# Kernel optimization log

Measured on AMD Instinct MI355X. Metric: run time of the kernel, lower is better.

Reference implementation:

```python
import jax, jax.numpy as jnp
import numpy as np

H = 8
D = 512
DK = D // H
B = 16
N = 8192


def setup_inputs() -> dict:
    key = jax.random.key(0)
    k1, k2, k3, k4 = jax.random.split(key, 4)
    x = jax.random.normal(k1, (B, N, D), dtype=jnp.float32)
    W_k = jax.random.normal(k2, (D, D), dtype=jnp.float32) * (1.0 / np.sqrt(D))
    W_g = jax.random.normal(k3, (D, D), dtype=jnp.float32) * (1.0 / np.sqrt(D))
    query = jax.random.normal(k4, (H, 1, DK), dtype=jnp.float32)
    return {"x": x, "W_k": W_k, "W_g": W_g, "query": query}


def reference(x, W_k, W_g, query):
    b, n, d = x.shape
    # nn.Linear: y = x @ W.T  (no bias)
    K = (x @ W_k.T).reshape(b, n, H, DK).transpose(0, 2, 1, 3)  # (b,h,n,dk)
    G = (x @ W_g.T).reshape(b, n, H, DK).transpose(0, 2, 1, 3)  # (b,h,n,dk)
    xh = x.reshape(b, n, H, DK).transpose(0, 2, 1, 3)           # (b,h,n,dk)
    gated = jnp.tanh(K) * jax.nn.sigmoid(G)                     # (b,h,n,dk)
    # single-query attention: scores (b,h,1,n)
    scores = jnp.einsum('hmd,bhnd->bhmn', query, gated)
    attn = jax.nn.softmax(scores, axis=-1)
    out = jnp.einsum('bhmn,bhnd->bhmd', attn, xh)               # (b,h,1,dk)
    out = out.transpose(0, 2, 1, 3).reshape(b, 1, H * DK)
    return out.squeeze()  # (b, d)
```

## Files before the change

### kernel.cpp

```cpp
#include <hip/hip_runtime.h>
#include <hip/hip_bf16.h>

#define H_ 8
#define D_ 512
#define DK_ 64
#define B_ 16
#define N_ 8192
#define M_ (B_ * N_)

typedef __attribute__((ext_vector_type(8))) short short8;
typedef __attribute__((ext_vector_type(4))) float floatx4;

__device__ __forceinline__ void glds16(const void* g, void* l) {
    __builtin_amdgcn_global_load_lds((const __attribute__((address_space(1))) void*)g,
                                     (__attribute__((address_space(3))) void*)l,
                                     16, 0, 0);
}

__device__ __forceinline__ unsigned short f2bf(float f) {
    unsigned u = __float_as_uint(f);
    return (unsigned short)((u + 0x7fffu + ((u >> 16) & 1u)) >> 16);
}

__device__ __forceinline__ unsigned cvt_pk(float lo, float hi) {
    unsigned r;
    asm("v_cvt_pk_bf16_f32 %0, %1, %2" : "=v"(r) : "v"(lo), "v"(hi));
    return r;
}

__device__ __forceinline__ short8 pack_bf8(float4 lo, float4 hi) {
    union { unsigned u[4]; short8 s; } tmp;
    tmp.u[0] = cvt_pk(lo.x, lo.y);
    tmp.u[1] = cvt_pk(lo.z, lo.w);
    tmp.u[2] = cvt_pk(hi.x, hi.y);
    tmp.u[3] = cvt_pk(hi.z, hi.w);
    return tmp.s;
}

#define NX4_ ((M_ * D_) / 4)
#define NW4_ ((D_ * D_) / 4)
__global__ __launch_bounds__(256) void cvt3_kernel(
    const float* __restrict__ x, const float* __restrict__ wk, const float* __restrict__ wg,
    unsigned short* __restrict__ xb, unsigned short* __restrict__ wkb, unsigned short* __restrict__ wgb) {
    int i = blockIdx.x * blockDim.x + threadIdx.x;
    const int stride = gridDim.x * blockDim.x;
    const int total = NX4_ + 2 * NW4_;
    for (; i < total; i += stride) {
        const float4* src;
        ushort4* dst;
        if (i < NX4_)              { src = (const float4*)x  + i;             dst = (ushort4*)xb  + i; }
        else if (i < NX4_ + NW4_)  { src = (const float4*)wk + (i - NX4_);    dst = (ushort4*)wkb + (i - NX4_); }
        else                       { src = (const float4*)wg + (i - NX4_ - NW4_); dst = (ushort4*)wgb + (i - NX4_ - NW4_); }
        float4 v = *src;
        ushort4 o;
        o.x = f2bf(v.x); o.y = f2bf(v.y); o.z = f2bf(v.z); o.w = f2bf(v.w);
        *dst = o;
    }
}

__global__ __launch_bounds__(256) void cvt_kernel(const float* __restrict__ src,
                                                  unsigned short* __restrict__ dst, int n4) {
    int i = blockIdx.x * blockDim.x + threadIdx.x;
    int stride = gridDim.x * blockDim.x;
    for (; i < n4; i += stride) {
        float4 v = ((const float4*)src)[i];
        ushort4 o;
        o.x = f2bf(v.x); o.y = f2bf(v.y); o.z = f2bf(v.z); o.w = f2bf(v.w);
        ((ushort4*)dst)[i] = o;
    }
}

__global__ __launch_bounds__(256, 2) void gemm_score_kernel(
    const unsigned short* __restrict__ xb,
    const unsigned short* __restrict__ wkb,
    const unsigned short* __restrict__ wgb,
    const float* __restrict__ query,
    float* __restrict__ s_buf)
{
    __shared__ __attribute__((aligned(16))) unsigned short lds_a[2][128 * 64];
    __shared__ __attribute__((aligned(16))) unsigned short lds_k[128 * 64];
    __shared__ __attribute__((aligned(16))) unsigned short lds_g[128 * 64];

    const int t = threadIdx.x;
    const int lane = t & 63;
    const int wave = t >> 6;
    const int wm = wave >> 1, wn = wave & 1;
    const int fr = lane & 15;
    const int q4 = lane >> 4;
    const int sw = fr & 7;

    const int g = blockIdx.x;
    const int xcd = g & 7;
    const int s = g >> 3;
    const int jt = s & 3;
    const int mt = ((s >> 2) << 3) | xcd;
    const int jc = jt * 128;
    const int m0 = mt * 128;

    size_t aoff[4];
    int boff[4];
#pragma unroll
    for (int i = 0; i < 4; ++i) {
        int p = i * 256 + t;
        int r = p >> 3;
        int c = (p & 7) ^ (r & 7);
        aoff[i] = (size_t)(m0 + r) * 512 + c * 8;
        boff[i] = (jc + r) * 512 + c * 8;
    }

    floatx4 acc_k[4][4], acc_g[4][4];
#pragma unroll
    for (int i = 0; i < 4; ++i)
#pragma unroll
        for (int j = 0; j < 4; ++j) { acc_k[i][j] = (floatx4)0.f; acc_g[i][j] = (floatx4)0.f; }

#pragma unroll
    for (int i = 0; i < 4; ++i)
        glds16(xb + aoff[i], &lds_a[0][(size_t)(i * 256 + t) * 8]);
#pragma unroll
    for (int i = 0; i < 4; ++i) {
        glds16(wkb + boff[i], lds_k + (size_t)(i * 256 + t) * 8);
        glds16(wgb + boff[i], lds_g + (size_t)(i * 256 + t) * 8);
    }
    __syncthreads();

    for (int kt = 0; kt < 8; ++kt) {
        const int cur = kt & 1;
        const unsigned short* la = lds_a[cur];
        const int k1 = (kt + 1) * 64;

        if (kt < 7) {
#pragma unroll
            for (int i = 0; i < 4; ++i)
                glds16(xb + aoff[i] + k1, &lds_a[cur ^ 1][(size_t)(i * 256 + t) * 8]);
        }

#pragma unroll
        for (int kc = 0; kc < 2; ++kc) {
            short8 a[4], bk[4], bg[4];
#pragma unroll
            for (int mi = 0; mi < 4; ++mi) {
                int off = (wm * 64 + mi * 16 + fr) * 64 + (q4 ^ sw) * 8;
                a[mi] = *(const short8*)&la[off ^ (kc * 32)];
            }
#pragma unroll
            for (int ni = 0; ni < 4; ++ni) {
                int off = (wn * 64 + ni * 16 + fr) * 64 + (q4 ^ sw) * 8;
                bk[ni] = *(const short8*)&lds_k[off ^ (kc * 32)];
                bg[ni] = *(const short8*)&lds_g[off ^ (kc * 32)];
            }
#pragma unroll
            for (int mi = 0; mi < 4; ++mi)
#pragma unroll
                for (int ni = 0; ni < 4; ++ni) {
                    acc_k[mi][ni] = __builtin_amdgcn_mfma_f32_16x16x32_bf16(a[mi], bk[ni], acc_k[mi][ni], 0, 0, 0);
                    acc_g[mi][ni] = __builtin_amdgcn_mfma_f32_16x16x32_bf16(a[mi], bg[ni], acc_g[mi][ni], 0, 0, 0);
                }
        }

        if (kt < 7) {
            __syncthreads();
#pragma unroll
            for (int i = 0; i < 4; ++i) {
                glds16(wkb + boff[i] + k1, lds_k + (size_t)(i * 256 + t) * 8);
                glds16(wgb + boff[i] + k1, lds_g + (size_t)(i * 256 + t) * 8);
            }
            __syncthreads();
        }
    }

    const int h = jt * 2 + wn;
    float qv[4];
#pragma unroll
    for (int ni = 0; ni < 4; ++ni) qv[ni] = query[h * 64 + ni * 16 + fr];

#pragma unroll
    for (int mi = 0; mi < 4; ++mi) {
#pragma unroll
        for (int r = 0; r < 4; ++r) {
            float v = 0.f;
#pragma unroll
            for (int ni = 0; ni < 4; ++ni) {
                float kv = acc_k[mi][ni][r];
                float gv = acc_g[mi][ni][r];
                float e2k = fminf(__expf(2.f * kv), 1e18f);
                float eg  = fminf(__expf(gv),      1e18f);
                float num = (e2k - 1.f) * eg;
                float den = (e2k + 1.f) * (eg + 1.f);
                v += qv[ni] * num * __builtin_amdgcn_rcpf(den);
            }
            v += __shfl_xor(v, 1);
            v += __shfl_xor(v, 2);
            v += __shfl_xor(v, 4);
            v += __shfl_xor(v, 8);
            if (fr == 0) {
                int mg = m0 + wm * 64 + mi * 16 + q4 * 4 + r;
                int b = mg >> 13, n = mg & 8191;
                s_buf[((size_t)(b * 8 + h) << 13) + n] = v;
            }
        }
    }
}

__global__ __launch_bounds__(256, 2) void gemm_score_kernel_fb(
    const float* __restrict__ x,
    const unsigned short* __restrict__ wkb,
    const unsigned short* __restrict__ wgb,
    const float* __restrict__ query,
    float* __restrict__ s_buf)
{
    __shared__ __attribute__((aligned(16))) unsigned short lds_a[128 * 64];
    __shared__ __attribute__((aligned(16))) unsigned short lds_k[128 * 64];
    __shared__ __attribute__((aligned(16))) unsigned short lds_g[128 * 64];

    const int t = threadIdx.x;
    const int lane = t & 63;
    const int wave = t >> 6;
    const int wm = wave >> 1, wn = wave & 1;
    const int fr = lane & 15;
    const int q4 = lane >> 4;
    const int sw = fr & 7;

    const int g = blockIdx.x;
    const int xcd = g & 7;
    const int s = g >> 3;
    const int jt = s & 3;
    const int mt = ((s >> 2) << 3) | xcd;
    const int jc = jt * 128;
    const int m0 = mt * 128;

    const int ar = t >> 3;
    const int ac = t & 7;
    const float* pA = x + (size_t)(m0 + ar) * 512 + ac * 8;
    const int awoff = ar * 64 + (ac ^ (ar & 7)) * 8;

    int boff[4];
#pragma unroll
    for (int i = 0; i < 4; ++i) {
        int p = i * 256 + t;
        int r = p >> 3;
        int c = (p & 7) ^ (r & 7);
        boff[i] = (jc + r) * 512 + c * 8;
    }

    floatx4 acc_k[4][4], acc_g[4][4];
#pragma unroll
    for (int i = 0; i < 4; ++i)
#pragma unroll
        for (int j = 0; j < 4; ++j) { acc_k[i][j] = (floatx4)0.f; acc_g[i][j] = (floatx4)0.f; }

    for (int k0 = 0; k0 < 512; k0 += 64) {
#pragma unroll
        for (int i = 0; i < 4; ++i) {
            glds16(wkb + boff[i] + k0, lds_k + (size_t)(i * 256 + t) * 8);
            glds16(wgb + boff[i] + k0, lds_g + (size_t)(i * 256 + t) * 8);
        }
        float4 av[8];
#pragma unroll
        for (int it = 0; it < 4; ++it) {
            const float* p = pA + (size_t)it * (32 * 512) + k0;
            av[it * 2]     = *(const float4*)(p);
            av[it * 2 + 1] = *(const float4*)(p + 4);
        }
#pragma unroll
        for (int it = 0; it < 4; ++it)
            *(short8*)&lds_a[it * (32 * 64) + awoff] = pack_bf8(av[it * 2], av[it * 2 + 1]);
        __syncthreads();

#pragma unroll
        for (int kc = 0; kc < 2; ++kc) {
            short8 a[4], bk[4], bg[4];
#pragma unroll
            for (int mi = 0; mi < 4; ++mi) {
                int off = (wm * 64 + mi * 16 + fr) * 64 + (q4 ^ sw) * 8;
                a[mi] = *(const short8*)&lds_a[off ^ (kc * 32)];
            }
#pragma unroll
            for (int ni = 0; ni < 4; ++ni) {
                int off = (wn * 64 + ni * 16 + fr) * 64 + (q4 ^ sw) * 8;
                bk[ni] = *(const short8*)&lds_k[off ^ (kc * 32)];
                bg[ni] = *(const short8*)&lds_g[off ^ (kc * 32)];
            }
#pragma unroll
            for (int mi = 0; mi < 4; ++mi)
#pragma unroll
                for (int ni = 0; ni < 4; ++ni) {
                    acc_k[mi][ni] = __builtin_amdgcn_mfma_f32_16x16x32_bf16(a[mi], bk[ni], acc_k[mi][ni], 0, 0, 0);
                    acc_g[mi][ni] = __builtin_amdgcn_mfma_f32_16x16x32_bf16(a[mi], bg[ni], acc_g[mi][ni], 0, 0, 0);
                }
        }
        __syncthreads();
    }

    const int h = jt * 2 + wn;
    float qv[4];
#pragma unroll
    for (int ni = 0; ni < 4; ++ni) qv[ni] = query[h * 64 + ni * 16 + fr];

#pragma unroll
    for (int mi = 0; mi < 4; ++mi) {
#pragma unroll
        for (int r = 0; r < 4; ++r) {
            float v = 0.f;
#pragma unroll
            for (int ni = 0; ni < 4; ++ni) {
                float kv = acc_k[mi][ni][r];
                float gv = acc_g[mi][ni][r];
                float e2k = fminf(__expf(2.f * kv), 1e18f);
                float eg  = fminf(__expf(gv),      1e18f);
                float num = (e2k - 1.f) * eg;
                float den = (e2k + 1.f) * (eg + 1.f);
                v += qv[ni] * num * __builtin_amdgcn_rcpf(den);
            }
            v += __shfl_xor(v, 1);
            v += __shfl_xor(v, 2);
            v += __shfl_xor(v, 4);
            v += __shfl_xor(v, 8);
            if (fr == 0) {
                int mg = m0 + wm * 64 + mi * 16 + q4 * 4 + r;
                int b = mg >> 13, n = mg & 8191;
                s_buf[((size_t)(b * 8 + h) << 13) + n] = v;
            }
        }
    }
}

__global__ __launch_bounds__(256) void stats_kernel(const float* __restrict__ s_buf,
                                                    float* __restrict__ mb, float* __restrict__ lb) {
    const int bh = blockIdx.x;
    const float4* s4 = (const float4*)(s_buf + ((size_t)bh << 13));
    const int t = threadIdx.x;
    float4 vv[8];
    float mx = -3.0e38f;
#pragma unroll
    for (int i = 0; i < 8; ++i) {
        float4 v = s4[t + i * 256];
        vv[i] = v;
        mx = fmaxf(mx, fmaxf(fmaxf(v.x, v.y), fmaxf(v.z, v.w)));
    }
#pragma unroll
    for (int m = 32; m > 0; m >>= 1) mx = fmaxf(mx, __shfl_xor(mx, m));
    __shared__ float red[8];
    if ((t & 63) == 0) red[t >> 6] = mx;
    __syncthreads();
    mx = fmaxf(fmaxf(red[0], red[1]), fmaxf(red[2], red[3]));
    float sum = 0.f;
#pragma unroll
    for (int i = 0; i < 8; ++i) {
        float4 v = vv[i];
        sum += __expf(v.x - mx) + __expf(v.y - mx) + __expf(v.z - mx) + __expf(v.w - mx);
    }
#pragma unroll
    for (int m = 32; m > 0; m >>= 1) sum += __shfl_xor(sum, m);
    if ((t & 63) == 0) red[4 + (t >> 6)] = sum;
    __syncthreads();
    if (t == 0) { mb[bh] = mx; lb[bh] = 1.f / (red[4] + red[5] + red[6] + red[7]); }
}

__global__ __launch_bounds__(256) void out_kernel(
    const float* __restrict__ x, const float* __restrict__ s_buf,
    const float* __restrict__ mb, const float* __restrict__ lb,
    float* __restrict__ out) {
    const int b = blockIdx.x >> 6;
    const int chunk = blockIdx.x & 63;
    const int n0 = chunk * 128;
    const int t = threadIdx.x;
    __shared__ float w[8 * 128];
    __shared__ float red[3 * 512];
    for (int i = t; i < 1024; i += 256) {
        int hh = i >> 7, nn = i & 127;
        int bh = b * 8 + hh;
        w[i] = __expf(s_buf[((size_t)bh << 13) + n0 + nn] - mb[bh]) * lb[bh];
    }
    __syncthreads();
    const int rg = t >> 6;
    const int d0 = (t & 63) * 8;
    const float* wh = w + ((d0 >> 6) << 7);
    const float* xb = x + (((size_t)(b * 8192 + n0)) << 9) + d0;
    float acc[8] = {0.f, 0.f, 0.f, 0.f, 0.f, 0.f, 0.f, 0.f};
    for (int i = 0; i < 32; i += 2) {
        const int n1 = rg + i * 4;
        const int n2 = n1 + 4;
        const float4* r1p = (const float4*)(xb + ((size_t)n1 << 9));
        const float4* r2p = (const float4*)(xb + ((size_t)n2 << 9));
        float4 a0 = r1p[0];
        float4 a1 = r1p[1];
        float4 b0 = r2p[0];
        float4 b1 = r2p[1];
        float w1 = wh[n1];
        float w2 = wh[n2];
        acc[0] += w1 * a0.x; acc[1] += w1 * a0.y; acc[2] += w1 * a0.z; acc[3] += w1 * a0.w;
        acc[4] += w1 * a1.x; acc[5] += w1 * a1.y; acc[6] += w1 * a1.z; acc[7] += w1 * a1.w;
        acc[0] += w2 * b0.x; acc[1] += w2 * b0.y; acc[2] += w2 * b0.z; acc[3] += w2 * b0.w;
        acc[4] += w2 * b1.x; acc[5] += w2 * b1.y; acc[6] += w2 * b1.z; acc[7] += w2 * b1.w;
    }
    if (rg != 0) {
#pragma unroll
        for (int j = 0; j < 8; ++j) red[(rg - 1) * 512 + (t & 63) * 8 + j] = acc[j];
    }
    __syncthreads();
    if (rg == 0) {
#pragma unroll
        for (int j = 0; j < 8; ++j) {
            float v = acc[j] + red[(t & 63) * 8 + j] + red[512 + (t & 63) * 8 + j]
                    + red[1024 + (t & 63) * 8 + j];
            atomicAdd(&out[b * 512 + d0 + j], v);
        }
    }
}

extern "C" void kernel_launch(void* const* d_in, const int* in_sizes, int n_in,
                              void* d_out, int out_size, void* d_ws, size_t ws_size,
                              hipStream_t stream) {
    const float* x  = (const float*)d_in[0];
    const float* Wk = (const float*)d_in[1];
    const float* Wg = (const float*)d_in[2];
    const float* q  = (const float*)d_in[3];
    float* out = (float*)d_out;

    char* ws = (char*)d_ws;
    unsigned short* wkb = (unsigned short*)ws;
    unsigned short* wgb = (unsigned short*)(ws + 524288ull);
    float* s_buf = (float*)(ws + 1048576ull);
    float* mb = (float*)(ws + 5242880ull);
    float* lb = (float*)(ws + 5243392ull);
    unsigned short* xb = (unsigned short*)(ws + (8ull << 20));

    const bool big_ws = ws_size >= (136ull << 20);

    hipMemsetAsync(d_out, 0, 512 * B_ * sizeof(float), stream);

    if (big_ws) {
        hipLaunchKernelGGL(cvt3_kernel, dim3(2048), dim3(256), 0, stream, x, Wk, Wg, xb, wkb, wgb);
        hipLaunchKernelGGL(gemm_score_kernel, dim3(4096), dim3(256), 0, stream, xb, wkb, wgb, q, s_buf);
    } else {
        hipLaunchKernelGGL(cvt_kernel, dim3(256), dim3(256), 0, stream, Wk, wkb, (D_ * D_) / 4);
        hipLaunchKernelGGL(cvt_kernel, dim3(256), dim3(256), 0, stream, Wg, wgb, (D_ * D_) / 4);
        hipLaunchKernelGGL(gemm_score_kernel_fb, dim3(4096), dim3(256), 0, stream, x, wkb, wgb, q, s_buf);
    }
    hipLaunchKernelGGL(stats_kernel, dim3(128), dim3(256), 0, stream, s_buf, mb, lb);
    hipLaunchKernelGGL(out_kernel, dim3(1024), dim3(256), 0, stream, x, s_buf, mb, lb, out);
}
```

Baseline: 594.7 us.

## Enlarge GEMM-score tile to 256 rows with 8 waves and pipelined staging

Rewrites the fused K/G GEMM + score kernel to use 512-thread blocks computing 256x128 tiles, double-buffering both A and the weight tiles and interleaving global-to-LDS prefetch with MFMA phases, using explicit barriers and setprio. The per-block head partial sums are combined through LDS before writing scores. The conversion kernel is also restructured with dedicated blocks per tensor and hardware packed bf16 conversion. The aim is higher weight reuse, fewer global loads and better overlap of loads with MFMA. The cost is more LDS (128KB per block) and possible occupancy or register pressure.

```diff
diff --git a/kernel.cpp b/kernel.cpp
--- a/kernel.cpp
+++ b/kernel.cpp
@@ -42,20 +42,197 @@
 __global__ __launch_bounds__(256) void cvt3_kernel(
     const float* __restrict__ x, const float* __restrict__ wk, const float* __restrict__ wg,
     unsigned short* __restrict__ xb, unsigned short* __restrict__ wkb, unsigned short* __restrict__ wgb) {
-    int i = blockIdx.x * blockDim.x + threadIdx.x;
-    const int stride = gridDim.x * blockDim.x;
-    const int total = NX4_ + 2 * NW4_;
-    for (; i < total; i += stride) {
-        const float4* src;
-        ushort4* dst;
-        if (i < NX4_)              { src = (const float4*)x  + i;             dst = (ushort4*)xb  + i; }
-        else if (i < NX4_ + NW4_)  { src = (const float4*)wk + (i - NX4_);    dst = (ushort4*)wkb + (i - NX4_); }
-        else                       { src = (const float4*)wg + (i - NX4_ - NW4_); dst = (ushort4*)wgb + (i - NX4_ - NW4_); }
-        float4 v = *src;
-        ushort4 o;
-        o.x = f2bf(v.x); o.y = f2bf(v.y); o.z = f2bf(v.z); o.w = f2bf(v.w);
-        *dst = o;
-    }
+    const int blk = blockIdx.x;
+    if (blk < 2048) {
+        const float4* src = (const float4*)x;
+        uint2* dst = (uint2*)xb;
+        int i = blk * 256 + threadIdx.x;
+#pragma unroll 4
+        for (int it = 0; it < 32; ++it, i += 524288) {
+            float4 v = src[i];
+            uint2 o;
+            o.x = cvt_pk(v.x, v.y);
+            o.y = cvt_pk(v.z, v.w);
+            dst[i] = o;
+        }
+    } else {
+        const bool is_k = blk < 2056;
+        const float4* src = (const float4*)(is_k ? wk : wg);
+        uint2* dst = (uint2*)(is_k ? wkb : wgb);
+        int base = ((blk - 2048) & 7) * 256 + threadIdx.x;
+#pragma unroll 4
+        for (int it = 0; it < 32; ++it) {
+            int i = base + it * 2048;
+            float4 v = src[i];
+            uint2 o;
+            o.x = cvt_pk(v.x, v.y);
+            o.y = cvt_pk(v.z, v.w);
+            dst[i] = o;
+        }
+    }
+}
+
+__global__ __launch_bounds__(512, 2) void gemm_score_kernel(
+    const unsigned short* __restrict__ xb,
+    const unsigned short* __restrict__ wkb,
+    const unsigned short* __restrict__ wgb,
+    const float* __restrict__ query,
+    float* __restrict__ s_buf)
+{
+    __shared__ __attribute__((aligned(16))) unsigned short lds_a[2][256 * 64];
+    __shared__ __attribute__((aligned(16))) unsigned short lds_b[2][256 * 64];
+
+    const int t = threadIdx.x;
+    const int lane = t & 63;
+    const int wave = t >> 6;
+    const int wm = wave >> 2;
+    const int wn = wave & 3;
+    const int fr = lane & 15;
+    const int q4 = lane >> 4;
+    const int sw = fr & 7;
+
+    const int g = blockIdx.x;
+    const int xcd = g & 7;
+    const int s = g >> 3;
+    const int jt = s & 3;
+    const int mt = ((s >> 2) << 3) | xcd;
+    const int jc = jt * 128;
+    const int m0 = mt * 256;
+
+    const unsigned short* asrc[2];
+    const unsigned short* bksrc[2];
+    const unsigned short* bgsrc[2];
+    int ldso[2];
+#pragma unroll
+    for (int i = 0; i < 2; ++i) {
+        int si = i * 512 + t;
+        int rl = si >> 3;
+        int c  = (si & 7) ^ (rl & 7);
+        asrc[i]  = xb  + (size_t)(m0 + rl) * 512 + c * 8;
+        bksrc[i] = wkb + (jc + rl) * 512 + c * 8;
+        bgsrc[i] = wgb + (jc + rl) * 512 + c * 8;
+        ldso[i] = si * 8;
+    }
+
+#define STAGE_AH(buf, h, k0) do { \
+        glds16(asrc[0] + (h) * (128 * 512) + (k0), &lds_a[buf][(h) * 8192 + ldso[0]]); \
+        glds16(asrc[1] + (h) * (128 * 512) + (k0), &lds_a[buf][(h) * 8192 + ldso[1]]); } while (0)
+#define STAGE_BK(buf, k0) do { \
+        glds16(bksrc[0] + (k0), &lds_b[buf][ldso[0]]); \
+        glds16(bksrc[1] + (k0), &lds_b[buf][ldso[1]]); } while (0)
+#define STAGE_BG(buf, k0) do { \
+        glds16(bgsrc[0] + (k0), &lds_b[buf][8192 + ldso[0]]); \
+        glds16(bgsrc[1] + (k0), &lds_b[buf][8192 + ldso[1]]); } while (0)
+
+    floatx4 acc_k[8][2], acc_g[8][2];
+#pragma unroll
+    for (int mi = 0; mi < 8; ++mi)
+#pragma unroll
+        for (int ni = 0; ni < 2; ++ni) { acc_k[mi][ni] = (floatx4)0.f; acc_g[mi][ni] = (floatx4)0.f; }
+
+    STAGE_AH(0, 0, 0); STAGE_AH(0, 1, 0); STAGE_BK(0, 0); STAGE_BG(0, 0);
+    __builtin_amdgcn_sched_barrier(0);
+    asm volatile("s_waitcnt vmcnt(0)" ::: "memory");
+    __builtin_amdgcn_s_barrier();
+
+#pragma unroll 2
+    for (int kt = 0; kt < 8; ++kt) {
+        const int cur = kt & 1, nxt = cur ^ 1;
+        const unsigned short* la = lds_a[cur];
+        const unsigned short* lb = lds_b[cur];
+        const int k1 = (kt + 1) * 64;
+        short8 bk[2][2], bg[2][2];
+
+#pragma unroll
+        for (int p = 0; p < 4; ++p) {
+            short8 a2[2][2];
+#pragma unroll
+            for (int e = 0; e < 2; ++e) {
+                int row = wm * 128 + (p * 2 + e) * 16 + fr;
+                int off = row * 64 + (q4 ^ sw) * 8;
+                a2[e][0] = *(const short8*)&la[off];
+                a2[e][1] = *(const short8*)&la[off ^ 32];
+            }
+            if (p == 0) {
+#pragma unroll
+                for (int ni = 0; ni < 2; ++ni) {
+                    int vk = (wn * 32 + ni * 16 + fr) * 64 + (q4 ^ sw) * 8;
+                    bk[ni][0] = *(const short8*)&lb[vk];
+                    bk[ni][1] = *(const short8*)&lb[vk ^ 32];
+                    bg[ni][0] = *(const short8*)&lb[vk + 8192];
+                    bg[ni][1] = *(const short8*)&lb[(vk ^ 32) + 8192];
+                }
+            }
+            if (kt < 7) {
+                if (p == 0) STAGE_AH(nxt, 0, k1);
+                if (p == 1) STAGE_AH(nxt, 1, k1);
+                if (p == 2) STAGE_BK(nxt, k1);
+                if (p == 3) STAGE_BG(nxt, k1);
+            }
+            __builtin_amdgcn_s_barrier();
+            asm volatile("s_waitcnt lgkmcnt(0)" ::: "memory");
+            __builtin_amdgcn_sched_barrier(0);
+            __builtin_amdgcn_s_setprio(1);
+#pragma unroll
+            for (int e = 0; e < 2; ++e) {
+                const int mi = p * 2 + e;
+#pragma unroll
+                for (int ni = 0; ni < 2; ++ni)
+#pragma unroll
+                    for (int kk = 0; kk < 2; ++kk) {
+                        acc_k[mi][ni] = __builtin_amdgcn_mfma_f32_16x16x32_bf16(a2[e][kk], bk[ni][kk], acc_k[mi][ni], 0, 0, 0);
+                        acc_g[mi][ni] = __builtin_amdgcn_mfma_f32_16x16x32_bf16(a2[e][kk], bg[ni][kk], acc_g[mi][ni], 0, 0, 0);
+                    }
+            }
+            __builtin_amdgcn_s_setprio(0);
+            if (p < 3) __builtin_amdgcn_s_barrier();
+        }
+        __builtin_amdgcn_sched_barrier(0);
+        if (kt < 7) asm volatile("s_waitcnt vmcnt(0)" ::: "memory");
+        __builtin_amdgcn_s_barrier();
+    }
+
+    float* part = (float*)&lds_a[0][0];
+    const int h = jt * 2 + (wn >> 1);
+    float qv[2];
+    qv[0] = query[h * 64 + (wn & 1) * 32 + fr];
+    qv[1] = query[h * 64 + (wn & 1) * 32 + 16 + fr];
+
+#pragma unroll
+    for (int mi = 0; mi < 8; ++mi) {
+#pragma unroll
+        for (int r = 0; r < 4; ++r) {
+            float v = 0.f;
+#pragma unroll
+            for (int ni = 0; ni < 2; ++ni) {
+                float kv = acc_k[mi][ni][r];
+                float gv = acc_g[mi][ni][r];
+                float e2k = fminf(__expf(2.f * kv), 1e18f);
+                float eg  = fminf(__expf(gv),      1e18f);
+                float num = (e2k - 1.f) * eg;
+                float den = (e2k + 1.f) * (eg + 1.f);
+                v += qv[ni] * num * __builtin_amdgcn_rcpf(den);
+            }
+            v += __shfl_xor(v, 1);
+            v += __shfl_xor(v, 2);
+            v += __shfl_xor(v, 4);
+            v += __shfl_xor(v, 8);
+            if (fr == 0)
+                part[wn * 256 + wm * 128 + mi * 16 + q4 * 4 + r] = v;
+        }
+    }
+    __syncthreads();
+    {
+        const int pr = t >> 8;
+        const int row = t & 255;
+        float val = part[(pr * 2) * 256 + row] + part[(pr * 2 + 1) * 256 + row];
+        int m = m0 + row;
+        int b = m >> 13, n = m & 8191;
+        s_buf[((size_t)(b * 8 + jt * 2 + pr) << 13) + n] = val;
+    }
+#undef STAGE_AH
+#undef STAGE_BK
+#undef STAGE_BG
 }
 
 __global__ __launch_bounds__(256) void cvt_kernel(const float* __restrict__ src,
@@ -67,138 +244,6 @@
         ushort4 o;
         o.x = f2bf(v.x); o.y = f2bf(v.y); o.z = f2bf(v.z); o.w = f2bf(v.w);
         ((ushort4*)dst)[i] = o;
-    }
-}
-
-__global__ __launch_bounds__(256, 2) void gemm_score_kernel(
-    const unsigned short* __restrict__ xb,
-    const unsigned short* __restrict__ wkb,
-    const unsigned short* __restrict__ wgb,
-    const float* __restrict__ query,
-    float* __restrict__ s_buf)
-{
-    __shared__ __attribute__((aligned(16))) unsigned short lds_a[2][128 * 64];
-    __shared__ __attribute__((aligned(16))) unsigned short lds_k[128 * 64];
-    __shared__ __attribute__((aligned(16))) unsigned short lds_g[128 * 64];
-
-    const int t = threadIdx.x;
-    const int lane = t & 63;
-    const int wave = t >> 6;
-    const int wm = wave >> 1, wn = wave & 1;
-    const int fr = lane & 15;
-    const int q4 = lane >> 4;
-    const int sw = fr & 7;
-
-    const int g = blockIdx.x;
-    const int xcd = g & 7;
-    const int s = g >> 3;
-    const int jt = s & 3;
-    const int mt = ((s >> 2) << 3) | xcd;
-    const int jc = jt * 128;
-    const int m0 = mt * 128;
-
-    size_t aoff[4];
-    int boff[4];
-#pragma unroll
-    for (int i = 0; i < 4; ++i) {
-        int p = i * 256 + t;
-        int r = p >> 3;
-        int c = (p & 7) ^ (r & 7);
-        aoff[i] = (size_t)(m0 + r) * 512 + c * 8;
-        boff[i] = (jc + r) * 512 + c * 8;
-    }
-
-    floatx4 acc_k[4][4], acc_g[4][4];
-#pragma unroll
-    for (int i = 0; i < 4; ++i)
-#pragma unroll
-        for (int j = 0; j < 4; ++j) { acc_k[i][j] = (floatx4)0.f; acc_g[i][j] = (floatx4)0.f; }
-
-#pragma unroll
-    for (int i = 0; i < 4; ++i)
-        glds16(xb + aoff[i], &lds_a[0][(size_t)(i * 256 + t) * 8]);
-#pragma unroll
-    for (int i = 0; i < 4; ++i) {
-        glds16(wkb + boff[i], lds_k + (size_t)(i * 256 + t) * 8);
-        glds16(wgb + boff[i], lds_g + (size_t)(i * 256 + t) * 8);
-    }
-    __syncthreads();
-
-    for (int kt = 0; kt < 8; ++kt) {
-        const int cur = kt & 1;
-        const unsigned short* la = lds_a[cur];
-        const int k1 = (kt + 1) * 64;
-
-        if (kt < 7) {
-#pragma unroll
-            for (int i = 0; i < 4; ++i)
-                glds16(xb + aoff[i] + k1, &lds_a[cur ^ 1][(size_t)(i * 256 + t) * 8]);
-        }
-
-#pragma unroll
-        for (int kc = 0; kc < 2; ++kc) {
-            short8 a[4], bk[4], bg[4];
-#pragma unroll
-            for (int mi = 0; mi < 4; ++mi) {
-                int off = (wm * 64 + mi * 16 + fr) * 64 + (q4 ^ sw) * 8;
-                a[mi] = *(const short8*)&la[off ^ (kc * 32)];
-            }
-#pragma unroll
-            for (int ni = 0; ni < 4; ++ni) {
-                int off = (wn * 64 + ni * 16 + fr) * 64 + (q4 ^ sw) * 8;
-                bk[ni] = *(const short8*)&lds_k[off ^ (kc * 32)];
-                bg[ni] = *(const short8*)&lds_g[off ^ (kc * 32)];
-            }
-#pragma unroll
-            for (int mi = 0; mi < 4; ++mi)
-#pragma unroll
-                for (int ni = 0; ni < 4; ++ni) {
-                    acc_k[mi][ni] = __builtin_amdgcn_mfma_f32_16x16x32_bf16(a[mi], bk[ni], acc_k[mi][ni], 0, 0, 0);
-                    acc_g[mi][ni] = __builtin_amdgcn_mfma_f32_16x16x32_bf16(a[mi], bg[ni], acc_g[mi][ni], 0, 0, 0);
-                }
-        }
-
-        if (kt < 7) {
-            __syncthreads();
-#pragma unroll
-            for (int i = 0; i < 4; ++i) {
-                glds16(wkb + boff[i] + k1, lds_k + (size_t)(i * 256 + t) * 8);
-                glds16(wgb + boff[i] + k1, lds_g + (size_t)(i * 256 + t) * 8);
-            }
-            __syncthreads();
-        }
-    }
-
-    const int h = jt * 2 + wn;
-    float qv[4];
-#pragma unroll
-    for (int ni = 0; ni < 4; ++ni) qv[ni] = query[h * 64 + ni * 16 + fr];
-
-#pragma unroll
-    for (int mi = 0; mi < 4; ++mi) {
-#pragma unroll
-        for (int r = 0; r < 4; ++r) {
-            float v = 0.f;
-#pragma unroll
-            for (int ni = 0; ni < 4; ++ni) {
-                float kv = acc_k[mi][ni][r];
-                float gv = acc_g[mi][ni][r];
-                float e2k = fminf(__expf(2.f * kv), 1e18f);
-                float eg  = fminf(__expf(gv),      1e18f);
-                float num = (e2k - 1.f) * eg;
-                float den = (e2k + 1.f) * (eg + 1.f);
-                v += qv[ni] * num * __builtin_amdgcn_rcpf(den);
-            }
-            v += __shfl_xor(v, 1);
-            v += __shfl_xor(v, 2);
-            v += __shfl_xor(v, 4);
-            v += __shfl_xor(v, 8);
-            if (fr == 0) {
-                int mg = m0 + wm * 64 + mi * 16 + q4 * 4 + r;
-                int b = mg >> 13, n = mg & 8191;
-                s_buf[((size_t)(b * 8 + h) << 13) + n] = v;
-            }
-        }
     }
 }
 
@@ -376,13 +421,13 @@
     const int rg = t >> 6;
     const int d0 = (t & 63) * 8;
     const float* wh = w + ((d0 >> 6) << 7);
-    const float* xb = x + (((size_t)(b * 8192 + n0)) << 9) + d0;
+    const float* xp = x + (((size_t)(b * 8192 + n0)) << 9) + d0;
     float acc[8] = {0.f, 0.f, 0.f, 0.f, 0.f, 0.f, 0.f, 0.f};
     for (int i = 0; i < 32; i += 2) {
         const int n1 = rg + i * 4;
         const int n2 = n1 + 4;
-        const float4* r1p = (const float4*)(xb + ((size_t)n1 << 9));
-        const float4* r2p = (const float4*)(xb + ((size_t)n2 << 9));
+        const float4* r1p = (const float4*)(xp + ((size_t)n1 << 9));
+        const float4* r2p = (const float4*)(xp + ((size_t)n2 << 9));
         float4 a0 = r1p[0];
         float4 a1 = r1p[1];
         float4 b0 = r2p[0];
@@ -431,8 +476,8 @@
     hipMemsetAsync(d_out, 0, 512 * B_ * sizeof(float), stream);
 
     if (big_ws) {
-        hipLaunchKernelGGL(cvt3_kernel, dim3(2048), dim3(256), 0, stream, x, Wk, Wg, xb, wkb, wgb);
-        hipLaunchKernelGGL(gemm_score_kernel, dim3(4096), dim3(256), 0, stream, xb, wkb, wgb, q, s_buf);
+        hipLaunchKernelGGL(cvt3_kernel, dim3(2064), dim3(256), 0, stream, x, Wk, Wg, xb, wkb, wgb);
+        hipLaunchKernelGGL(gemm_score_kernel, dim3(2048), dim3(512), 0, stream, xb, wkb, wgb, q, s_buf);
     } else {
         hipLaunchKernelGGL(cvt_kernel, dim3(256), dim3(256), 0, stream, Wk, wkb, (D_ * D_) / 4);
         hipLaunchKernelGGL(cvt_kernel, dim3(256), dim3(256), 0, stream, Wg, wgb, (D_ * D_) / 4);
```

Measured after the change: 634.0 us. +6.6%, slower.
